# Kernel tuning notes

Hardware: AMD Instinct MI355X
Metric: run time of the kernel (lower is better)

Reference implementation:

```python
import jax, jax.numpy as jnp
import numpy as np

B, C, N = 8, 256, 4096

def setup_inputs() -> dict:
    key = jax.random.key(0)
    k1, k2, k3 = jax.random.split(key, 3)
    pts_feat = jax.random.normal(k1, (B, C, N), dtype=jnp.float32)
    # Conv1d(channels, channels, 1, bias=False) weight is [C_out, C_in, 1] -> store as [C_out, C_in]
    scale = 1.0 / np.sqrt(C)
    Wq = jax.random.uniform(k2, (C, C), dtype=jnp.float32, minval=-scale, maxval=scale)
    Wk = jax.random.uniform(k3, (C, C), dtype=jnp.float32, minval=-scale, maxval=scale)
    return {"pts_feat": pts_feat, "Wq": Wq, "Wk": Wk}

def reference(pts_feat, Wq, Wk):
    # 1x1 conv == channel-wise matmul. x_q: [B, N, C], x_k: [B, C, N]
    x_q = jnp.einsum('bcn,dc->bnd', pts_feat, Wq)
    x_k = jnp.einsum('bcn,dc->bdn', pts_feat, Wk)
    logits = jnp.einsum('bnc,bcm->bnm', x_q, x_k)          # [B, N, N]
    attn = jax.nn.softmax(logits, axis=-1)
    attn = attn / (1e-8 + attn.sum(axis=-1, keepdims=True))
    # torch.einsum('bnn,bnc->bnc', attn, feat) takes the DIAGONAL of attn
    # and scales each point's raw feature vector by it (no contraction).
    diag = jnp.diagonal(attn, axis1=1, axis2=2)            # [B, N]
    x_attn = pts_feat * diag[:, None, :]                   # [B, C, N]
    return x_attn
```

## Files before the change

### kernel.cpp

```cpp
#include <hip/hip_runtime.h>
#include <hip/hip_bf16.h>
#include <cstdint>

#define B_ 8
#define C_ 256
#define N_ 4096

typedef __bf16 bf16;
typedef __bf16 bf16x8 __attribute__((ext_vector_type(8)));
typedef float f32x4 __attribute__((ext_vector_type(4)));
typedef unsigned int u32;

__device__ __forceinline__ void async_ld16(const void* g, void* l) {
  __builtin_amdgcn_global_load_lds(
      (const __attribute__((address_space(1))) void*)g,
      (__attribute__((address_space(3))) void*)l, 16, 0, 0);
}

__device__ __forceinline__ float bh2f(unsigned short u) {
  union { u32 i; float f; } x; x.i = ((u32)u) << 16; return x.f;
}
__device__ __forceinline__ unsigned short f2bh(float f) {
  union { float f; u32 i; } x; x.f = f;
  u32 i = x.i + 0x7fffu + ((x.i >> 16) & 1u);
  return (unsigned short)(i >> 16);
}

__device__ __forceinline__ bool wave_sniff_fp32(const unsigned short* p) {
  int l = threadIdx.x & 63;
  unsigned short u = p[2 * l];
  int e = (u >> 7) & 0xff;
  unsigned long long m = __ballot(e >= 112 && e <= 142);
  return __popcll(m) < 32;
}

__global__ __launch_bounds__(256) void k_wconv(const void* __restrict__ Wv,
                                               unsigned short* __restrict__ Wc) {
  bool f32 = wave_sniff_fp32((const unsigned short*)Wv);
  int i = (blockIdx.x * 256 + threadIdx.x) * 4;
  if (f32) {
    float4 v = *(const float4*)((const float*)Wv + i);
    unsigned short o0 = f2bh(v.x), o1 = f2bh(v.y), o2 = f2bh(v.z), o3 = f2bh(v.w);
    uint2 o; o.x = ((u32)o1 << 16) | o0; o.y = ((u32)o3 << 16) | o2;
    *(uint2*)(Wc + i) = o;
  } else {
    uint2 v = *(const uint2*)((const unsigned short*)Wv + i);
    *(uint2*)(Wc + i) = v;
  }
}

__global__ __launch_bounds__(256) void k_transpose(const void* __restrict__ Fv,
                                                   unsigned short* __restrict__ Ft) {
  bool f32 = wave_sniff_fp32((const unsigned short*)Fv);
  __shared__ unsigned short tile[64 * 66];
  int n0 = blockIdx.x * 64, c0 = blockIdx.y * 64, b = blockIdx.z;
  int t = threadIdx.x;
#pragma unroll
  for (int p = 0; p < 2; ++p) {
    int c = (t >> 3) + 32 * p;
    int n = (t & 7) * 8;
    size_t off = (size_t)(b * C_ + c0 + c) * N_ + n0 + n;
    unsigned short vals[8];
    if (f32) {
      const float* src = (const float*)Fv + off;
      float4 v0 = *(const float4*)(src);
      float4 v1 = *(const float4*)(src + 4);
      vals[0] = f2bh(v0.x); vals[1] = f2bh(v0.y); vals[2] = f2bh(v0.z); vals[3] = f2bh(v0.w);
      vals[4] = f2bh(v1.x); vals[5] = f2bh(v1.y); vals[6] = f2bh(v1.z); vals[7] = f2bh(v1.w);
    } else {
      uint4 v = *(const uint4*)((const unsigned short*)Fv + off);
      vals[0] = (unsigned short)(v.x & 0xffffu); vals[1] = (unsigned short)(v.x >> 16);
      vals[2] = (unsigned short)(v.y & 0xffffu); vals[3] = (unsigned short)(v.y >> 16);
      vals[4] = (unsigned short)(v.z & 0xffffu); vals[5] = (unsigned short)(v.z >> 16);
      vals[6] = (unsigned short)(v.w & 0xffffu); vals[7] = (unsigned short)(v.w >> 16);
    }
#pragma unroll
    for (int s = 0; s < 8; ++s) tile[c * 66 + n + s] = vals[s];
  }
  __syncthreads();
#pragma unroll
  for (int p = 0; p < 4; ++p) {
    int n = (t >> 4) + 16 * p;
    int cq = (t & 15) * 4;
    unsigned short e0 = tile[(cq + 0) * 66 + n];
    unsigned short e1 = tile[(cq + 1) * 66 + n];
    unsigned short e2 = tile[(cq + 2) * 66 + n];
    unsigned short e3 = tile[(cq + 3) * 66 + n];
    uint2 o;
    o.x = ((u32)e1 << 16) | e0;
    o.y = ((u32)e3 << 16) | e2;
    *(uint2*)(Ft + ((size_t)(b * N_ + n0 + n) * C_ + c0 + cq)) = o;
  }
}

__global__ __launch_bounds__(256) void k_proj(const bf16* __restrict__ Ft,
                                              const bf16* __restrict__ Wq,
                                              const bf16* __restrict__ Wk,
                                              bf16* __restrict__ Qt,
                                              bf16* __restrict__ Kt) {
  __shared__ bf16 As[128 * 32];
  __shared__ bf16 Bs[128 * 32];
  int n0 = blockIdx.x * 128;
  int b = blockIdx.y;
  int z = blockIdx.z;
  int d0 = (z & 1) * 128;
  const bf16* W = (z >> 1) ? Wk : Wq;
  bf16* Dst = (z >> 1) ? Kt : Qt;
  int t = threadIdx.x;
  int w = t >> 6, l = t & 63;
  int wm = (w & 1) * 64, wn = (w >> 1) * 64;
  int lr = l & 15, lq = l >> 4;
  const size_t fbase = (size_t)b * N_ * C_;

  f32x4 acc[4][4] = {};
  for (int kc = 0; kc < 8; ++kc) {
    __syncthreads();
#pragma unroll
    for (int r = 0; r < 2; ++r) {
      int ci = r * 4 + w;
      int e = ci * 64 + l;
      int row = e >> 2, coff = (e & 3) * 8;
      async_ld16(Ft + fbase + (size_t)(n0 + row) * C_ + kc * 32 + coff, As + ci * 512);
      async_ld16(W + (size_t)(d0 + row) * C_ + kc * 32 + coff, Bs + ci * 512);
    }
    __syncthreads();
    bf16x8 a[4], bb[4];
#pragma unroll
    for (int i = 0; i < 4; ++i)
      a[i] = *(const bf16x8*)(As + (wm + 16 * i + lr) * 32 + lq * 8);
#pragma unroll
    for (int j = 0; j < 4; ++j)
      bb[j] = *(const bf16x8*)(Bs + (wn + 16 * j + lr) * 32 + lq * 8);
#pragma unroll
    for (int i = 0; i < 4; ++i)
#pragma unroll
      for (int j = 0; j < 4; ++j)
        acc[i][j] = __builtin_amdgcn_mfma_f32_16x16x32_bf16(a[i], bb[j], acc[i][j], 0, 0, 0);
  }
#pragma unroll
  for (int i = 0; i < 4; ++i)
#pragma unroll
    for (int j = 0; j < 4; ++j)
#pragma unroll
      for (int r = 0; r < 4; ++r) {
        int row = n0 + wm + 16 * i + lq * 4 + r;
        int col = d0 + wn + 16 * j + lr;
        Dst[fbase + (size_t)row * C_ + col] = (bf16)acc[i][j][r];
      }
}

__global__ __launch_bounds__(256, 2) void k_attn(const bf16* __restrict__ Qt,
                                                 const bf16* __restrict__ Kt,
                                                 float* __restrict__ snn,
                                                 float* __restrict__ lsum) {
  __shared__ bf16 Ks[8 * 128 * 32];
  __shared__ float rs[2][128];
  int ntile = blockIdx.x, b = blockIdx.y, h = blockIdx.z;
  int n0 = ntile * 128;
  int t = threadIdx.x, w = t >> 6, l = t & 63;
  int wm = (w & 1) * 64, wn = (w >> 1) * 64;
  int lr = l & 15, lq = l >> 4;
  const size_t gbase = (size_t)b * N_ * C_;

  bf16x8 a[4][8];
#pragma unroll
  for (int i = 0; i < 4; ++i)
#pragma unroll
    for (int kc = 0; kc < 8; ++kc)
      a[i][kc] = *(const bf16x8*)(Qt + gbase + (size_t)(n0 + wm + 16 * i + lr) * C_ + kc * 32 + lq * 8);

  float part[16];
#pragma unroll
  for (int s = 0; s < 16; ++s) part[s] = 0.f;

  int m_base = h * 2048;
  bool has_diag = (n0 >= m_base) && (n0 < m_base + 2048);
  int diag_it = ntile & 15;

  for (int it = 0; it < 16; ++it) {
    int m0 = m_base + it * 128;
    __syncthreads();
#pragma unroll
    for (int u = 0; u < 16; ++u) {
      int unit = u * 4 + w;
      int kc = unit >> 3, ci = unit & 7;
      int e = ci * 64 + l;
      int row = e >> 2, coff = (e & 3) * 8;
      async_ld16(Kt + gbase + (size_t)(m0 + row) * C_ + kc * 32 + coff,
                 Ks + kc * 4096 + ci * 512);
    }
    __syncthreads();
    f32x4 acc[4][4] = {};
#pragma unroll
    for (int kc = 0; kc < 8; ++kc) {
      bf16x8 bb[4];
#pragma unroll
      for (int j = 0; j < 4; ++j)
        bb[j] = *(const bf16x8*)(Ks + kc * 4096 + (wn + 16 * j + lr) * 32 + lq * 8);
#pragma unroll
      for (int i = 0; i < 4; ++i)
#pragma unroll
        for (int j = 0; j < 4; ++j)
          acc[i][j] = __builtin_amdgcn_mfma_f32_16x16x32_bf16(a[i][kc], bb[j], acc[i][j], 0, 0, 0);
    }
    bool dit = has_diag && (it == diag_it);
#pragma unroll
    for (int i = 0; i < 4; ++i)
#pragma unroll
      for (int j = 0; j < 4; ++j)
#pragma unroll
        for (int r = 0; r < 4; ++r) {
          float e = __expf(acc[i][j][r]);
          part[i * 4 + r] += e;
          if (dit) {
            int rloc = wm + 16 * i + lq * 4 + r;
            int cloc = wn + 16 * j + lr;
            if (rloc == cloc) snn[b * N_ + n0 + rloc] = e;
          }
        }
  }

#pragma unroll
  for (int s = 0; s < 16; ++s) {
    float v = part[s];
    v += __shfl_xor(v, 1);
    v += __shfl_xor(v, 2);
    v += __shfl_xor(v, 4);
    v += __shfl_xor(v, 8);
    part[s] = v;
  }
  if (lr == 0) {
#pragma unroll
    for (int i = 0; i < 4; ++i)
#pragma unroll
      for (int r = 0; r < 4; ++r)
        rs[w >> 1][wm + 16 * i + lq * 4 + r] = part[i * 4 + r];
  }
  __syncthreads();
  if (t < 128) {
    float lv = rs[0][t] + rs[1][t];
    lsum[((size_t)h * B_ + b) * N_ + n0 + t] = lv;
  }
}

__global__ __launch_bounds__(256) void k_diag(const float* __restrict__ snn,
                                              const float* __restrict__ lsum,
                                              float* __restrict__ diag) {
  int i = blockIdx.x * 256 + threadIdx.x;
  float lv = lsum[i] + lsum[(size_t)B_ * N_ + i];
  diag[i] = snn[i] / (lv * (1.0f + 1e-8f));
}

__global__ __launch_bounds__(256) void k_scale(const void* __restrict__ Fv,
                                               const float* __restrict__ diag,
                                               void* __restrict__ Outv) {
  bool f32 = wave_sniff_fp32((const unsigned short*)Fv);
  int g = blockIdx.x * 256 + threadIdx.x;
  size_t base = (size_t)g * 8;
  int n = (int)(base & (N_ - 1));
  int b = (int)(base >> 20);
  float4 d0 = *(const float4*)(diag + (size_t)b * N_ + n);
  float4 d1 = *(const float4*)(diag + (size_t)b * N_ + n + 4);
  float dd[8] = {d0.x, d0.y, d0.z, d0.w, d1.x, d1.y, d1.z, d1.w};
  if (f32) {
    const float* F = (const float*)Fv + base;
    float* O = (float*)Outv + base;
    float4 a0 = *(const float4*)(F);
    float4 a1 = *(const float4*)(F + 4);
    float4 o0, o1;
    o0.x = a0.x * dd[0]; o0.y = a0.y * dd[1]; o0.z = a0.z * dd[2]; o0.w = a0.w * dd[3];
    o1.x = a1.x * dd[4]; o1.y = a1.y * dd[5]; o1.z = a1.z * dd[6]; o1.w = a1.w * dd[7];
    *(float4*)(O) = o0;
    *(float4*)(O + 4) = o1;
  } else {
    uint4 v = *(const uint4*)((const unsigned short*)Fv + base);
    u32 vv[4] = {v.x, v.y, v.z, v.w};
    u32 o[4];
#pragma unroll
    for (int k = 0; k < 4; ++k) {
      float lo = bh2f((unsigned short)(vv[k] & 0xffffu)) * dd[2 * k];
      float hi = bh2f((unsigned short)(vv[k] >> 16)) * dd[2 * k + 1];
      o[k] = ((u32)f2bh(hi) << 16) | f2bh(lo);
    }
    uint4 ov; ov.x = o[0]; ov.y = o[1]; ov.z = o[2]; ov.w = o[3];
    *(uint4*)((unsigned short*)Outv + base) = ov;
  }
}

extern "C" void kernel_launch(void* const* d_in, const int* in_sizes, int n_in,
                              void* d_out, int out_size, void* d_ws, size_t ws_size,
                              hipStream_t stream) {
  (void)in_sizes; (void)n_in; (void)out_size; (void)ws_size;
  const void* F = d_in[0];
  const void* Wq = d_in[1];
  const void* Wk = d_in[2];
  char* ws = (char*)d_ws;
  bf16* Ft = (bf16*)(ws);
  bf16* Qt = (bf16*)(ws + (16u << 20));
  bf16* Kt = (bf16*)(ws + (32u << 20));
  char* tail = ws + (48u << 20);
  float* snn = (float*)(tail);
  float* lsum = (float*)(tail + 131072);
  float* diag = (float*)(tail + 131072 + 262144);
  bf16* Wqc = (bf16*)(tail + 131072 + 262144 + 131072);
  bf16* Wkc = (bf16*)(tail + 131072 + 262144 + 131072 + 131072);

  k_wconv<<<64, 256, 0, stream>>>(Wq, (unsigned short*)Wqc);
  k_wconv<<<64, 256, 0, stream>>>(Wk, (unsigned short*)Wkc);
  k_transpose<<<dim3(N_ / 64, C_ / 64, B_), 256, 0, stream>>>(F, (unsigned short*)Ft);
  k_proj<<<dim3(N_ / 128, B_, 4), 256, 0, stream>>>(Ft, Wqc, Wkc, Qt, Kt);
  k_attn<<<dim3(N_ / 128, B_, 2), 256, 0, stream>>>(Qt, Kt, snn, lsum);
  k_diag<<<(B_ * N_) / 256, 256, 0, stream>>>(snn, lsum, diag);
  k_scale<<<(B_ * C_ * N_ / 8) / 256, 256, 0, stream>>>(F, diag, d_out);
}
```

Baseline: 206.3 us.

## Retile attention kernel for higher occupancy and fuse diag into scale kernel

The attention kernel now uses a 128x64 tile with each wave owning 32 rows, half the LDS, and launch bounds allowing 4 blocks per CU. It also uses a 1D grid ordered with batch and half as the fastest-varying indices. The separate diag normalization kernel is folded into the scale kernel, and the two weight-convert launches are merged into one. The aims are better latency hiding and fewer launches, at the cost of less K reuse per loaded tile.

```diff
diff --git a/kernel.cpp b/kernel.cpp
--- a/kernel.cpp
+++ b/kernel.cpp
@@ -34,8 +34,12 @@
   return __popcll(m) < 32;
 }
 
-__global__ __launch_bounds__(256) void k_wconv(const void* __restrict__ Wv,
-                                               unsigned short* __restrict__ Wc) {
+__global__ __launch_bounds__(256) void k_wconv(const void* __restrict__ W0,
+                                               const void* __restrict__ W1,
+                                               unsigned short* __restrict__ Wc0,
+                                               unsigned short* __restrict__ Wc1) {
+  const void* Wv = blockIdx.y ? W1 : W0;
+  unsigned short* Wc = blockIdx.y ? Wc1 : Wc0;
   bool f32 = wave_sniff_fp32((const unsigned short*)Wv);
   int i = (blockIdx.x * 256 + threadIdx.x) * 4;
   if (f32) {
@@ -149,63 +153,60 @@
       }
 }
 
-__global__ __launch_bounds__(256, 2) void k_attn(const bf16* __restrict__ Qt,
+__global__ __launch_bounds__(256, 4) void k_attn(const bf16* __restrict__ Qt,
                                                  const bf16* __restrict__ Kt,
                                                  float* __restrict__ snn,
                                                  float* __restrict__ lsum) {
-  __shared__ bf16 Ks[8 * 128 * 32];
-  __shared__ float rs[2][128];
-  int ntile = blockIdx.x, b = blockIdx.y, h = blockIdx.z;
+  __shared__ bf16 Ks[8 * 64 * 32];
+  int bid = blockIdx.x;
+  int b = bid & 7, h = (bid >> 3) & 1, ntile = bid >> 4;
   int n0 = ntile * 128;
   int t = threadIdx.x, w = t >> 6, l = t & 63;
-  int wm = (w & 1) * 64, wn = (w >> 1) * 64;
   int lr = l & 15, lq = l >> 4;
+  int wrow = w * 32;
   const size_t gbase = (size_t)b * N_ * C_;
 
-  bf16x8 a[4][8];
-#pragma unroll
-  for (int i = 0; i < 4; ++i)
+  bf16x8 a[2][8];
+#pragma unroll
+  for (int i = 0; i < 2; ++i)
 #pragma unroll
     for (int kc = 0; kc < 8; ++kc)
-      a[i][kc] = *(const bf16x8*)(Qt + gbase + (size_t)(n0 + wm + 16 * i + lr) * C_ + kc * 32 + lq * 8);
-
-  float part[16];
-#pragma unroll
-  for (int s = 0; s < 16; ++s) part[s] = 0.f;
+      a[i][kc] = *(const bf16x8*)(Qt + gbase + (size_t)(n0 + wrow + 16 * i + lr) * C_ + kc * 32 + lq * 8);
+
+  float part[8];
+#pragma unroll
+  for (int s = 0; s < 8; ++s) part[s] = 0.f;
 
   int m_base = h * 2048;
-  bool has_diag = (n0 >= m_base) && (n0 < m_base + 2048);
-  int diag_it = ntile & 15;
-
-  for (int it = 0; it < 16; ++it) {
-    int m0 = m_base + it * 128;
+  bool has_diag = ((ntile >> 4) == h);
+  int d0 = (ntile & 15) * 2;
+
+  int srow = t >> 2, scoff = (t & 3) * 8;
+
+  for (int it = 0; it < 32; ++it) {
+    int m0 = m_base + it * 64;
     __syncthreads();
 #pragma unroll
-    for (int u = 0; u < 16; ++u) {
-      int unit = u * 4 + w;
-      int kc = unit >> 3, ci = unit & 7;
-      int e = ci * 64 + l;
-      int row = e >> 2, coff = (e & 3) * 8;
-      async_ld16(Kt + gbase + (size_t)(m0 + row) * C_ + kc * 32 + coff,
-                 Ks + kc * 4096 + ci * 512);
-    }
+    for (int kc = 0; kc < 8; ++kc)
+      async_ld16(Kt + gbase + (size_t)(m0 + srow) * C_ + kc * 32 + scoff,
+                 Ks + kc * 2048 + t * 8);
     __syncthreads();
-    f32x4 acc[4][4] = {};
+    f32x4 acc[2][4] = {};
 #pragma unroll
     for (int kc = 0; kc < 8; ++kc) {
       bf16x8 bb[4];
 #pragma unroll
       for (int j = 0; j < 4; ++j)
-        bb[j] = *(const bf16x8*)(Ks + kc * 4096 + (wn + 16 * j + lr) * 32 + lq * 8);
-#pragma unroll
-      for (int i = 0; i < 4; ++i)
+        bb[j] = *(const bf16x8*)(Ks + kc * 2048 + (16 * j + lr) * 32 + lq * 8);
+#pragma unroll
+      for (int i = 0; i < 2; ++i)
 #pragma unroll
         for (int j = 0; j < 4; ++j)
           acc[i][j] = __builtin_amdgcn_mfma_f32_16x16x32_bf16(a[i][kc], bb[j], acc[i][j], 0, 0, 0);
     }
-    bool dit = has_diag && (it == diag_it);
-#pragma unroll
-    for (int i = 0; i < 4; ++i)
+    bool dit = has_diag && ((it >> 1) == (ntile & 15));
+#pragma unroll
+    for (int i = 0; i < 2; ++i)
 #pragma unroll
       for (int j = 0; j < 4; ++j)
 #pragma unroll
@@ -213,15 +214,15 @@
           float e = __expf(acc[i][j][r]);
           part[i * 4 + r] += e;
           if (dit) {
-            int rloc = wm + 16 * i + lq * 4 + r;
-            int cloc = wn + 16 * j + lr;
-            if (rloc == cloc) snn[b * N_ + n0 + rloc] = e;
+            int rloc = wrow + 16 * i + lq * 4 + r;
+            int cloc = 16 * j + lr;
+            if ((it - d0) * 64 + cloc == rloc) snn[b * N_ + n0 + rloc] = e;
           }
         }
   }
 
 #pragma unroll
-  for (int s = 0; s < 16; ++s) {
+  for (int s = 0; s < 8; ++s) {
     float v = part[s];
     v += __shfl_xor(v, 1);
     v += __shfl_xor(v, 2);
@@ -231,37 +232,38 @@
   }
   if (lr == 0) {
 #pragma unroll
-    for (int i = 0; i < 4; ++i)
+    for (int i = 0; i < 2; ++i)
 #pragma unroll
       for (int r = 0; r < 4; ++r)
-        rs[w >> 1][wm + 16 * i + lq * 4 + r] = part[i * 4 + r];
-  }
-  __syncthreads();
-  if (t < 128) {
-    float lv = rs[0][t] + rs[1][t];
-    lsum[((size_t)h * B_ + b) * N_ + n0 + t] = lv;
-  }
-}
-
-__global__ __launch_bounds__(256) void k_diag(const float* __restrict__ snn,
-                                              const float* __restrict__ lsum,
-                                              float* __restrict__ diag) {
-  int i = blockIdx.x * 256 + threadIdx.x;
-  float lv = lsum[i] + lsum[(size_t)B_ * N_ + i];
-  diag[i] = snn[i] / (lv * (1.0f + 1e-8f));
+        lsum[((size_t)h * B_ + b) * N_ + n0 + wrow + 16 * i + lq * 4 + r] = part[i * 4 + r];
+  }
 }
 
 __global__ __launch_bounds__(256) void k_scale(const void* __restrict__ Fv,
-                                               const float* __restrict__ diag,
+                                               const float* __restrict__ snn,
+                                               const float* __restrict__ lsum,
                                                void* __restrict__ Outv) {
   bool f32 = wave_sniff_fp32((const unsigned short*)Fv);
   int g = blockIdx.x * 256 + threadIdx.x;
   size_t base = (size_t)g * 8;
   int n = (int)(base & (N_ - 1));
   int b = (int)(base >> 20);
-  float4 d0 = *(const float4*)(diag + (size_t)b * N_ + n);
-  float4 d1 = *(const float4*)(diag + (size_t)b * N_ + n + 4);
-  float dd[8] = {d0.x, d0.y, d0.z, d0.w, d1.x, d1.y, d1.z, d1.w};
+  float4 s0 = *(const float4*)(snn + (size_t)b * N_ + n);
+  float4 s1 = *(const float4*)(snn + (size_t)b * N_ + n + 4);
+  float4 l00 = *(const float4*)(lsum + (size_t)b * N_ + n);
+  float4 l01 = *(const float4*)(lsum + (size_t)b * N_ + n + 4);
+  float4 l10 = *(const float4*)(lsum + (size_t)(B_ + b) * N_ + n);
+  float4 l11 = *(const float4*)(lsum + (size_t)(B_ + b) * N_ + n + 4);
+  const float c1 = 1.0f + 1e-8f;
+  float dd[8];
+  dd[0] = s0.x / ((l00.x + l10.x) * c1);
+  dd[1] = s0.y / ((l00.y + l10.y) * c1);
+  dd[2] = s0.z / ((l00.z + l10.z) * c1);
+  dd[3] = s0.w / ((l00.w + l10.w) * c1);
+  dd[4] = s1.x / ((l01.x + l11.x) * c1);
+  dd[5] = s1.y / ((l01.y + l11.y) * c1);
+  dd[6] = s1.z / ((l01.z + l11.z) * c1);
+  dd[7] = s1.w / ((l01.w + l11.w) * c1);
   if (f32) {
     const float* F = (const float*)Fv + base;
     float* O = (float*)Outv + base;
@@ -301,15 +303,12 @@
   char* tail = ws + (48u << 20);
   float* snn = (float*)(tail);
   float* lsum = (float*)(tail + 131072);
-  float* diag = (float*)(tail + 131072 + 262144);
-  bf16* Wqc = (bf16*)(tail + 131072 + 262144 + 131072);
-  bf16* Wkc = (bf16*)(tail + 131072 + 262144 + 131072 + 131072);
-
-  k_wconv<<<64, 256, 0, stream>>>(Wq, (unsigned short*)Wqc);
-  k_wconv<<<64, 256, 0, stream>>>(Wk, (unsigned short*)Wkc);
+  bf16* Wqc = (bf16*)(tail + 131072 + 262144);
+  bf16* Wkc = (bf16*)(tail + 131072 + 262144 + 131072);
+
+  k_wconv<<<dim3(64, 2), 256, 0, stream>>>(Wq, Wk, (unsigned short*)Wqc, (unsigned short*)Wkc);
   k_transpose<<<dim3(N_ / 64, C_ / 64, B_), 256, 0, stream>>>(F, (unsigned short*)Ft);
   k_proj<<<dim3(N_ / 128, B_, 4), 256, 0, stream>>>(Ft, Wqc, Wkc, Qt, Kt);
-  k_attn<<<dim3(N_ / 128, B_, 2), 256, 0, stream>>>(Qt, Kt, snn, lsum);
-  k_diag<<<(B_ * N_) / 256, 256, 0, stream>>>(snn, lsum, diag);
-  k_scale<<<(B_ * C_ * N_ / 8) / 256, 256, 0, stream>>>(F, diag, d_out);
-}
+  k_attn<<<512, 256, 0, stream>>>(Qt, Kt, snn, lsum);
+  k_scale<<<(B_ * C_ * N_ / 8) / 256, 256, 0, stream>>>(F, snn, lsum, d_out);
+}
```

Measured after the change: 189.3 us. 8.3% less time.
